# Kernel optimization log

Measured on AMD Instinct MI355X. Metric: run time of the kernel, lower is better.

Reference implementation:

```python
import jax, jax.numpy as jnp
import numpy as np

CODEBOOK_SIZE = 8192
TOKEN_SIZE = 256
COMMITMENT_COST = 0.25
B, C, H, W = 32, 256, 32, 32


def setup_inputs() -> dict:
    key = jax.random.key(0)
    k1, k2 = jax.random.split(key)
    z = jax.random.normal(k1, (B, C, H, W), dtype=jnp.float32)
    # torch init: uniform_(-1/codebook_size, 1/codebook_size)
    embedding = jax.random.uniform(
        k2, (CODEBOOK_SIZE, TOKEN_SIZE), dtype=jnp.float32,
        minval=-1.0 / CODEBOOK_SIZE, maxval=1.0 / CODEBOOK_SIZE)
    return {"z": z, "embedding": embedding}


def reference(z, embedding):
    # b c h w -> b h w c
    z = jnp.transpose(z.astype(jnp.float32), (0, 2, 3, 1))
    b, h, w, c = z.shape
    z_flat = z.reshape(-1, c)  # [N, c]

    # squared euclidean distances: ||z||^2 + ||e||^2 - 2 z e^T
    d = (jnp.sum(z_flat ** 2, axis=1, keepdims=True)
         + jnp.sum(embedding ** 2, axis=1)
         - 2.0 * jnp.einsum('nd,kd->nk', z_flat, embedding))  # [N, K]
    idx = jnp.argmin(d, axis=1)  # [N]

    z_q = embedding[idx].reshape(z.shape)  # [b,h,w,c]

    commitment_loss = COMMITMENT_COST * jnp.mean(
        (jax.lax.stop_gradient(z_q) - z) ** 2)
    codebook_loss = jnp.mean((z_q - jax.lax.stop_gradient(z)) ** 2)
    loss = commitment_loss + codebook_loss

    # straight-through estimator
    z_q_st = z + jax.lax.stop_gradient(z_q - z)
    z_q_out = jnp.transpose(z_q_st, (0, 3, 1, 2))  # b h w c -> b c h w

    min_encoding_indices = idx.reshape(b, h, w)
    return (z_q_out, loss, commitment_loss, codebook_loss,
            min_encoding_indices)
```

## Files before the change

### kernel.cpp

```cpp
#include <hip/hip_runtime.h>
#include <float.h>

#define NBATCH 32
#define NCHAN  256
#define NHW    1024
#define NTOK   32768
#define NK     8192
#define ND     256
#define ZELEMS 8388608
#define OUT_LOSS 8388608
#define OUT_IDX  8388611
#define MARGIN   1.2e-4f

typedef short bf16x8  __attribute__((ext_vector_type(8)));
typedef float f32x4   __attribute__((ext_vector_type(4)));
typedef float f32x16  __attribute__((ext_vector_type(16)));

__device__ __forceinline__ unsigned short f2bf(float f) {
    unsigned int u = __float_as_uint(f);
    u += 0x7FFFu + ((u >> 16) & 1u);
    return (unsigned short)(u >> 16);
}

__device__ __forceinline__ float embed8(float x, int code) {
    return __int_as_float((__float_as_int(x) & 0xFFFFFF00) | code);
}


__global__ __launch_bounds__(256) void k_cast(const float* __restrict__ zg,
                                              const float* __restrict__ E,
                                              unsigned short* __restrict__ Epre,
                                              unsigned short* __restrict__ Zpre,
                                              float* __restrict__ en,
                                              float* __restrict__ acc,
                                              int* __restrict__ counter) {
    __shared__ unsigned short buf[128][34];
    const int t = threadIdx.x;
    if (blockIdx.x < 1024) {
        int g = blockIdx.x * 256 + t;
        int code = g >> 5, c16 = g & 31;
        int kc = c16 >> 2, ks = (c16 >> 1) & 1, lhi = c16 & 1;
        const float4* E4 = (const float4*)(E + code * ND + c16 * 8);
        float4 a = E4[0], b = E4[1];
        float s = a.x*a.x + a.y*a.y + a.z*a.z + a.w*a.w
                + b.x*b.x + b.y*b.y + b.z*b.z + b.w*b.w;
        #pragma unroll
        for (int off = 1; off < 32; off <<= 1) s += __shfl_xor(s, off, 64);
        if ((t & 31) == 0) en[code] = s;
        unsigned int u[4];
        u[0] = (unsigned int)f2bf(a.x) | ((unsigned int)f2bf(a.y) << 16);
        u[1] = (unsigned int)f2bf(a.z) | ((unsigned int)f2bf(a.w) << 16);
        u[2] = (unsigned int)f2bf(b.x) | ((unsigned int)f2bf(b.y) << 16);
        u[3] = (unsigned int)f2bf(b.z) | ((unsigned int)f2bf(b.w) << 16);
        *(uint4*)((char*)Epre + (size_t)(code >> 7) * 65536 + kc * 8192
                  + (ks * 2 + lhi) * 2048 + (code & 127) * 16) =
            make_uint4(u[0], u[1], u[2], u[3]);
        if (blockIdx.x == 0 && t == 0) { acc[0] = 0.0f; counter[0] = 0; }
    } else {
        int bi = blockIdx.x - 1024;
        int b = bi >> 6, kc = (bi >> 3) & 7, hwt = bi & 7;
        int c0 = kc * 32, hw0 = hwt * 128;
        #pragma unroll
        for (int r = 0; r < 4; ++r) {
            int idx = r * 256 + t;
            int c = idx >> 5, q = idx & 31;
            float4 v = *(const float4*)&zg[(b * 256 + c0 + c) * 1024 + hw0 + q * 4];
            buf[q * 4 + 0][c] = f2bf(v.x);
            buf[q * 4 + 1][c] = f2bf(v.y);
            buf[q * 4 + 2][c] = f2bf(v.z);
            buf[q * 4 + 3][c] = f2bf(v.w);
        }
        __syncthreads();
        int tok = t >> 1, ks = t & 1;
        char* base = (char*)Zpre + (size_t)((b * 8 + hwt) * 8 + kc) * 8192;
        #pragma unroll
        for (int lhi = 0; lhi < 2; ++lhi) {
            unsigned int u[4];
            #pragma unroll
            for (int k = 0; k < 4; ++k) {
                int cc = ks * 16 + lhi * 8 + 2 * k;
                u[k] = (unsigned int)buf[tok][cc] | ((unsigned int)buf[tok][cc + 1] << 16);
            }
            *(uint4*)(base + (ks * 2 + lhi) * 2048 + tok * 16) =
                make_uint4(u[0], u[1], u[2], u[3]);
        }
    }
}

__global__ __launch_bounds__(256, 4) void k_dist(const unsigned short* __restrict__ Epre,
                                                 const unsigned short* __restrict__ Zpre,
                                                 const float* __restrict__ en,
                                                 float2* __restrict__ part2) {
    __shared__ float2 red[2][128];
    __shared__ float en_s[128];

    const int t    = threadIdx.x;
    const int kbb  = blockIdx.x;
    const int mb   = blockIdx.y;
    const int n0   = mb * 128;
    const int w    = t >> 6, lane = t & 63;
    const int l31  = lane & 31, lhi = lane >> 5;
    const int wm   = w >> 1, wn = w & 1;

    float en_v = (t < 128) ? en[kbb * 128 + t] : 0.0f;

    const char* Ep = (const char*)Epre + (size_t)kbb * 65536
                   + lhi * 2048 + (wm * 64 + l31) * 16;
    const char* Zp = (const char*)Zpre + (size_t)mb * 65536
                   + lhi * 2048 + (wn * 64 + l31) * 16;

    bf16x8 ea[2][2][2], zb[2][2][2];
    auto loadE = [&](int kc, int pp) {
        const char* p = Ep + kc * 8192;
        #pragma unroll
        for (int i = 0; i < 2; ++i)
            #pragma unroll
            for (int ks = 0; ks < 2; ++ks)
                ea[pp][i][ks] = *(const bf16x8*)(p + ks * 4096 + i * 512);
    };
    auto loadZ = [&](int kc, int pp) {
        const char* p = Zp + kc * 8192;
        #pragma unroll
        for (int j = 0; j < 2; ++j)
            #pragma unroll
            for (int ks = 0; ks < 2; ++ks)
                zb[pp][j][ks] = *(const bf16x8*)(p + ks * 4096 + j * 512);
    };

    f32x16 acc[2][2];
    #pragma unroll
    for (int i = 0; i < 2; ++i)
        #pragma unroll
        for (int j = 0; j < 2; ++j) acc[i][j] = (f32x16)0.0f;

    __builtin_amdgcn_s_setprio(1);
    loadE(0, 0);
    loadZ(0, 0);
    #pragma unroll
    for (int kc = 0; kc < 8; ++kc) {
        const int pp = kc & 1;
        if (kc < 7) { loadE(kc + 1, pp ^ 1); loadZ(kc + 1, pp ^ 1); }
        #pragma unroll
        for (int ks = 0; ks < 2; ++ks)
            #pragma unroll
            for (int i = 0; i < 2; ++i)
                #pragma unroll
                for (int j = 0; j < 2; ++j)
                    acc[i][j] = __builtin_amdgcn_mfma_f32_32x32x16_bf16(
                        ea[pp][i][ks], zb[pp][j][ks], acc[i][j], 0, 0, 0);
    }
    __builtin_amdgcn_s_setprio(0);

    if (t < 128) en_s[t] = en_v;
    __syncthreads();

    float v1[2] = { FLT_MAX, FLT_MAX }, v2[2] = { FLT_MAX, FLT_MAX };
    #pragma unroll
    for (int i = 0; i < 2; ++i) {
        const int cb = (wm << 6) | (i << 5) | (lhi << 2);
        #pragma unroll
        for (int rq = 0; rq < 4; ++rq) {
            f32x4 ev = *(const f32x4*)&en_s[cb + 8 * rq];
            #pragma unroll
            for (int rr = 0; rr < 4; ++rr) {
                const int r = rq * 4 + rr;
                const int code = cb + 8 * rq + rr;
                #pragma unroll
                for (int j = 0; j < 2; ++j) {
                    float s  = fmaf(-2.0f, acc[i][j][r], ev[rr]);
                    float se = embed8(s, code);
                    v2[j] = __builtin_amdgcn_fmed3f(se, v1[j], v2[j]);
                    v1[j] = fminf(v1[j], se);
                }
            }
        }
    }
    #pragma unroll
    for (int j = 0; j < 2; ++j) {
        float b1 = __shfl_xor(v1[j], 32, 64);
        float b2 = __shfl_xor(v2[j], 32, 64);
        float hi = fmaxf(v1[j], b1);
        v1[j] = fminf(v1[j], b1);
        v2[j] = fminf(fminf(hi, v2[j]), b2);
    }
    if (lane < 32) {
        #pragma unroll
        for (int j = 0; j < 2; ++j)
            red[wm][wn * 64 + j * 32 + lane] = make_float2(v1[j], v2[j]);
    }
    __syncthreads();
    if (t < 128) {
        float2 A = red[0][t], B = red[1][t];
        float g1 = fminf(A.x, B.x);
        float g2 = fminf(fminf(fmaxf(A.x, B.x), A.y), B.y);
        part2[(size_t)kbb * NTOK + n0 + t] = make_float2(g1, g2);
    }
}

__global__ __launch_bounds__(256) void k_refine(const float* __restrict__ zg,
                                                const float* __restrict__ E,
                                                const float2* __restrict__ part2,
                                                int* __restrict__ idxw,
                                                float* __restrict__ outF) {
    __shared__ float Zs[256 * 65];
    const int t = threadIdx.x;
    const int n0 = blockIdx.x * 64;
    const int b = n0 >> 10, hw0 = n0 & 1023;

    #pragma unroll
    for (int r = 0; r < 16; ++r) {
        int li = r * 256 + t;
        int c = li >> 4, q = li & 15;
        float4 v = *(const float4*)&zg[(b * 256 + c) * 1024 + hw0 + q * 4];
        Zs[c * 65 + q * 4 + 0] = v.x;
        Zs[c * 65 + q * 4 + 1] = v.y;
        Zs[c * 65 + q * 4 + 2] = v.z;
        Zs[c * 65 + q * 4 + 3] = v.w;
    }
    __syncthreads();

    const int w = t >> 6, l = t & 63;
    for (int it = 0; it < 16; ++it) {
        const int tokl = w * 16 + it;
        const int n = n0 + tokl;

        float zreg[4];
        #pragma unroll
        for (int j = 0; j < 4; ++j) zreg[j] = Zs[(64 * j + l) * 65 + tokl];

        double z2 = 0.0;
        #pragma unroll
        for (int j = 0; j < 4; ++j) z2 += (double)zreg[j] * (double)zreg[j];
        #pragma unroll
        for (int m = 1; m < 64; m <<= 1) z2 += __shfl_xor(z2, m, 64);
        const float z2f = (float)z2;

        float2 p = part2[(size_t)l * NTOK + n];
        int code1 = (l << 7) | (__float_as_int(p.x) & 0x7F);
        int code2 = (l << 7) | (__float_as_int(p.y) & 0x7F);

        float vmin = p.x;
        #pragma unroll
        for (int m = 1; m < 64; m <<= 1) vmin = fminf(vmin, __shfl_xor(vmin, m, 64));
        const float thr = vmin + MARGIN;

        unsigned long long m1 = __ballot(p.x <= thr);
        unsigned long long m2 = __ballot(p.y <= thr);

        float bdq = FLT_MAX; int bidx = 0x7fffffff;
        #pragma unroll
        for (int pass = 0; pass < 2; ++pass) {
            unsigned long long mm = pass ? m2 : m1;
            int ibits = pass ? code2 : code1;
            while (mm) {
                int src = __ffsll(mm) - 1; mm &= mm - 1;
                int cidx = __shfl(ibits, src, 64);
                const float* erow = E + cidx * ND;
                double g = (double)zreg[0] * (double)erow[l]
                         + (double)zreg[1] * (double)erow[64 + l]
                         + (double)zreg[2] * (double)erow[128 + l]
                         + (double)zreg[3] * (double)erow[192 + l];
                #pragma unroll
                for (int mk = 1; mk < 64; mk <<= 1) g += __shfl_xor(g, mk, 64);
                float c  = (float)(2.0 * g);
                float dq = z2f - c;
                if (dq < bdq || (dq == bdq && cidx < bidx)) { bdq = dq; bidx = cidx; }
            }
        }
        if (l == 0) { idxw[n] = bidx; outF[OUT_IDX + n] = (float)bidx; }
    }
}

__global__ __launch_bounds__(256) void k_gather(const float* __restrict__ E,
                                                const float* __restrict__ zg,
                                                const int* __restrict__ idxw,
                                                float* __restrict__ out,
                                                float* __restrict__ acc,
                                                int* __restrict__ counter) {
    __shared__ __align__(16) float Es[64 * 256];
    __shared__ int sidx[64];
    __shared__ float wred[4];
    const int t = threadIdx.x;
    const int b = blockIdx.x >> 4, ht = blockIdx.x & 15;

    if (t < 64) sidx[t] = idxw[b * 1024 + ht * 64 + t];
    __syncthreads();
    const float4* E4 = (const float4*)E;
    #pragma unroll
    for (int r = 0; r < 16; ++r) {
        int li = r * 256 + t;
        int row = li >> 6, slot = li & 63;
        float4 v = E4[(size_t)sidx[row] * 64 + slot];
        *(float4*)&Es[row * 256 + ((slot ^ (row & 15)) * 4)] = v;
    }
    __syncthreads();

    const int hw = t & 63, wv = t >> 6;
    float s = 0.0f;
    #pragma unroll 8
    for (int cc = 0; cc < 64; ++cc) {
        int c = wv * 64 + cc;
        float e = Es[hw * 256 + (((c >> 2) ^ (hw & 15)) * 4) + (c & 3)];
        size_t gi = (size_t)(b * 256 + c) * 1024 + ht * 64 + hw;
        float zv = zg[gi];
        out[gi] = e;
        float d = e - zv;
        s = fmaf(d, d, s);
    }
    #pragma unroll
    for (int off = 32; off > 0; off >>= 1) s += __shfl_down(s, off, 64);
    if ((t & 63) == 0) wred[wv] = s;
    __syncthreads();
    if (t == 0) {
        atomicAdd(acc, wred[0] + wred[1] + wred[2] + wred[3]);
        __threadfence();
        int old = atomicAdd(counter, 1);
        if (old == 511) {
            float total = atomicAdd(acc, 0.0f);
            float mse = total / 8388608.0f;
            out[OUT_LOSS + 0] = 1.25f * mse;
            out[OUT_LOSS + 1] = 0.25f * mse;
            out[OUT_LOSS + 2] = mse;
        }
    }
}

extern "C" void kernel_launch(void* const* d_in, const int* in_sizes, int n_in,
                              void* d_out, int out_size, void* d_ws, size_t ws_size,
                              hipStream_t stream) {
    const float* zg = (const float*)d_in[0];
    const float* E  = (const float*)d_in[1];
    float* out = (float*)d_out;
    float* wsf = (float*)d_ws;
    float*  acc     = wsf;
    int*    counter = (int*)(wsf + 1);
    float*  en      = wsf + 64;
    int*    idxw    = (int*)(wsf + 64 + NK);
    float2* part2   = (float2*)(wsf + 64 + NK + NTOK);
    unsigned short* Epre = (unsigned short*)(wsf + 64 + NK + NTOK + 4194304);
    unsigned short* Zpre = (unsigned short*)d_out;

    k_cast  <<<3072, 256, 0, stream>>>(zg, E, Epre, Zpre, en, acc, counter);
    k_dist  <<<dim3(64, 256), 256, 0, stream>>>(Epre, Zpre, en, part2);
    k_refine<<<NTOK / 64, 256, 0, stream>>>(zg, E, part2, idxw, out);
    k_gather<<<512, 256, 0, stream>>>(E, zg, idxw, out, acc, counter);
}
```

Baseline: 319.5 us.

## Stage k_dist tiles through LDS and widen codebook tile per block

k_dist now covers 256 codes per block instead of 128, which halves the grid width. Operand tiles are double-buffered into shared memory with global_load_lds, and the waves read their MFMA fragments from there instead of loading them straight from global memory. Each Z tile is therefore reused across twice as many codes, and the global fetch runs asynchronously while the MFMAs work on the other buffer. k_refine is changed to read 32 partial results per token and decode an 8-bit local code index. The cost is more accumulator registers, a lower occupancy target (2 blocks per CU instead of 4) and a barrier on every k-step.

```diff
diff --git a/kernel.cpp b/kernel.cpp
--- a/kernel.cpp
+++ b/kernel.cpp
@@ -87,77 +87,85 @@
     }
 }
 
-__global__ __launch_bounds__(256, 4) void k_dist(const unsigned short* __restrict__ Epre,
+__global__ __launch_bounds__(256, 2) void k_dist(const unsigned short* __restrict__ Epre,
                                                  const unsigned short* __restrict__ Zpre,
                                                  const float* __restrict__ en,
                                                  float2* __restrict__ part2) {
+    __shared__ __align__(16) char Elds[2][16384];
+    __shared__ __align__(16) char Zlds[2][8192];
     __shared__ float2 red[2][128];
-    __shared__ float en_s[128];
+    __shared__ float en_s[256];
 
     const int t    = threadIdx.x;
-    const int kbb  = blockIdx.x;
+    const int kbb2 = blockIdx.x;
     const int mb   = blockIdx.y;
     const int n0   = mb * 128;
     const int w    = t >> 6, lane = t & 63;
     const int l31  = lane & 31, lhi = lane >> 5;
     const int wm   = w >> 1, wn = w & 1;
 
-    float en_v = (t < 128) ? en[kbb * 128 + t] : 0.0f;
-
-    const char* Ep = (const char*)Epre + (size_t)kbb * 65536
-                   + lhi * 2048 + (wm * 64 + l31) * 16;
-    const char* Zp = (const char*)Zpre + (size_t)mb * 65536
-                   + lhi * 2048 + (wn * 64 + l31) * 16;
-
-    bf16x8 ea[2][2][2], zb[2][2][2];
-    auto loadE = [&](int kc, int pp) {
-        const char* p = Ep + kc * 8192;
-        #pragma unroll
-        for (int i = 0; i < 2; ++i)
-            #pragma unroll
-            for (int ks = 0; ks < 2; ++ks)
-                ea[pp][i][ks] = *(const bf16x8*)(p + ks * 4096 + i * 512);
+    const char* Esrc = (const char*)Epre + (size_t)kbb2 * 131072;
+    const char* Zsrc = (const char*)Zpre + (size_t)mb * 65536;
+
+    auto STAGE = [&](int bb, int kc) {
+        #pragma unroll
+        for (int s = 0; s < 2; ++s)
+            #pragma unroll
+            for (int h = 0; h < 2; ++h)
+                __builtin_amdgcn_global_load_lds(
+                    (const unsigned int*)(Esrc + (size_t)s * 65536 + kc * 8192 + h * 4096 + t * 16),
+                    (unsigned int*)&Elds[bb][s * 8192 + h * 4096 + t * 16], 16, 0, 0);
+        #pragma unroll
+        for (int h = 0; h < 2; ++h)
+            __builtin_amdgcn_global_load_lds(
+                (const unsigned int*)(Zsrc + kc * 8192 + h * 4096 + t * 16),
+                (unsigned int*)&Zlds[bb][h * 4096 + t * 16], 16, 0, 0);
     };
-    auto loadZ = [&](int kc, int pp) {
-        const char* p = Zp + kc * 8192;
-        #pragma unroll
-        for (int j = 0; j < 2; ++j)
-            #pragma unroll
-            for (int ks = 0; ks < 2; ++ks)
-                zb[pp][j][ks] = *(const bf16x8*)(p + ks * 4096 + j * 512);
-    };
-
-    f32x16 acc[2][2];
-    #pragma unroll
-    for (int i = 0; i < 2; ++i)
+
+    f32x16 acc[4][2];
+    #pragma unroll
+    for (int i = 0; i < 4; ++i)
         #pragma unroll
         for (int j = 0; j < 2; ++j) acc[i][j] = (f32x16)0.0f;
 
-    __builtin_amdgcn_s_setprio(1);
-    loadE(0, 0);
-    loadZ(0, 0);
+    STAGE(0, 0);
+    en_s[t] = en[kbb2 * 256 + t];
+    __syncthreads();
+
     #pragma unroll
     for (int kc = 0; kc < 8; ++kc) {
         const int pp = kc & 1;
-        if (kc < 7) { loadE(kc + 1, pp ^ 1); loadZ(kc + 1, pp ^ 1); }
+        if (kc < 7) STAGE(pp ^ 1, kc + 1);
+        const char* Eb = &Elds[pp][0] + wm * 8192 + lhi * 2048 + l31 * 16;
+        const char* Zb = &Zlds[pp][0] + lhi * 2048 + (wn * 64 + l31) * 16;
+        bf16x8 ea[4][2], zb[2][2];
+        #pragma unroll
+        for (int i = 0; i < 4; ++i)
+            #pragma unroll
+            for (int ks = 0; ks < 2; ++ks)
+                ea[i][ks] = *(const bf16x8*)(Eb + ks * 4096 + i * 512);
+        #pragma unroll
+        for (int j = 0; j < 2; ++j)
+            #pragma unroll
+            for (int ks = 0; ks < 2; ++ks)
+                zb[j][ks] = *(const bf16x8*)(Zb + ks * 4096 + j * 512);
+        __builtin_amdgcn_s_setprio(1);
         #pragma unroll
         for (int ks = 0; ks < 2; ++ks)
             #pragma unroll
-            for (int i = 0; i < 2; ++i)
+            for (int i = 0; i < 4; ++i)
                 #pragma unroll
                 for (int j = 0; j < 2; ++j)
                     acc[i][j] = __builtin_amdgcn_mfma_f32_32x32x16_bf16(
-                        ea[pp][i][ks], zb[pp][j][ks], acc[i][j], 0, 0, 0);
-    }
-    __builtin_amdgcn_s_setprio(0);
-
-    if (t < 128) en_s[t] = en_v;
-    __syncthreads();
+                        ea[i][ks], zb[j][ks], acc[i][j], 0, 0, 0);
+        __builtin_amdgcn_s_setprio(0);
+        __syncthreads();
+    }
 
     float v1[2] = { FLT_MAX, FLT_MAX }, v2[2] = { FLT_MAX, FLT_MAX };
     #pragma unroll
-    for (int i = 0; i < 2; ++i) {
-        const int cb = (wm << 6) | (i << 5) | (lhi << 2);
+    for (int i = 0; i < 4; ++i) {
+        const int cb = wm * 128 + i * 32 + lhi * 4;
         #pragma unroll
         for (int rq = 0; rq < 4; ++rq) {
             f32x4 ev = *(const f32x4*)&en_s[cb + 8 * rq];
@@ -186,14 +194,14 @@
     if (lane < 32) {
         #pragma unroll
         for (int j = 0; j < 2; ++j)
-            red[wm][wn * 64 + j * 32 + lane] = make_float2(v1[j], v2[j]);
+            red[wm][wn * 64 + j * 32 + l31] = make_float2(v1[j], v2[j]);
     }
     __syncthreads();
     if (t < 128) {
         float2 A = red[0][t], B = red[1][t];
         float g1 = fminf(A.x, B.x);
         float g2 = fminf(fminf(fmaxf(A.x, B.x), A.y), B.y);
-        part2[(size_t)kbb * NTOK + n0 + t] = make_float2(g1, g2);
+        part2[(size_t)kbb2 * NTOK + n0 + t] = make_float2(g1, g2);
     }
 }
 
@@ -235,9 +243,10 @@
         for (int m = 1; m < 64; m <<= 1) z2 += __shfl_xor(z2, m, 64);
         const float z2f = (float)z2;
 
-        float2 p = part2[(size_t)l * NTOK + n];
-        int code1 = (l << 7) | (__float_as_int(p.x) & 0x7F);
-        int code2 = (l << 7) | (__float_as_int(p.y) & 0x7F);
+        float2 p = make_float2(FLT_MAX, FLT_MAX);
+        if (l < 32) p = part2[(size_t)l * NTOK + n];
+        int code1 = (l << 8) | (__float_as_int(p.x) & 0xFF);
+        int code2 = (l << 8) | (__float_as_int(p.y) & 0xFF);
 
         float vmin = p.x;
         #pragma unroll
@@ -341,7 +350,7 @@
     unsigned short* Zpre = (unsigned short*)d_out;
 
     k_cast  <<<3072, 256, 0, stream>>>(zg, E, Epre, Zpre, en, acc, counter);
-    k_dist  <<<dim3(64, 256), 256, 0, stream>>>(Epre, Zpre, en, part2);
+    k_dist  <<<dim3(32, 256), 256, 0, stream>>>(Epre, Zpre, en, part2);
     k_refine<<<NTOK / 64, 256, 0, stream>>>(zg, E, part2, idxw, out);
     k_gather<<<512, 256, 0, stream>>>(E, zg, idxw, out, acc, counter);
 }
```

Measured after the change: 295.3 us. 1.08x faster.
